# Kernel tuning notes

Hardware: AMD Instinct MI355X
Metric: run time of the kernel (lower is better)

The kernel has to match this reference:

```python
import jax, jax.numpy as jnp
import numpy as np

B, S, E, H = 2, 2048, 1024, 16
D = E // H  # head_dim = 64


def setup_inputs() -> dict:
    key = jax.random.key(0)
    k1, k2, k3 = jax.random.split(key, 3)
    scale_in = 1.0 / np.sqrt(E)
    return {
        "x": jax.random.normal(k1, (B, S, E), dtype=jnp.float32),
        "mask": jnp.ones((B, S), dtype=jnp.int32),
        "qkv_w": jax.random.normal(k2, (3 * E, E), dtype=jnp.float32) * scale_in,
        "qkv_b": jnp.zeros((3 * E,), dtype=jnp.float32),
        "proj_w": jax.random.normal(k3, (E, E), dtype=jnp.float32) * scale_in,
        "proj_b": jnp.zeros((E,), dtype=jnp.float32),
    }


def reference(x, mask, qkv_w, qkv_b, proj_w, proj_b):
    b, s, e = x.shape
    # fused QKV projection: torch Linear -> x @ W^T + b
    qkv = x @ qkv_w.T + qkv_b                      # [B,S,3E]
    qkv = qkv.reshape(b, s, 3, H, D).transpose(2, 0, 3, 1, 4)  # [3,B,H,S,D]
    q, k, v = qkv[0], qkv[1], qkv[2]
    scores = jnp.einsum("bhqd,bhkd->bhqk", q, k) / jnp.sqrt(jnp.float32(D))
    # mask [B,S] -> [B,1,1,S]; masked_fill(mask==0, -inf)
    m = mask[:, None, None, :]
    scores = jnp.where(m == 0, -jnp.inf, scores)
    attn = jax.nn.softmax(scores, axis=-1)
    attn = jnp.nan_to_num(attn, nan=0.0)           # fully-masked rows -> 0
    # dropout is identity in eval mode (deterministic reference)
    out = jnp.einsum("bhqk,bhkd->bhqd", attn, v)   # [B,H,S,D]
    out = out.transpose(0, 2, 1, 3).reshape(b, s, e)
    out = out @ proj_w.T + proj_b
    return out
```

## Files before the change

### kernel.cpp

```cpp
#include <hip/hip_runtime.h>
#include <hip/hip_bf16.h>

#define B_ 2
#define S_ 2048
#define E_ 1024
#define H_ 16
#define D_ 64

typedef __bf16 bf16x8 __attribute__((ext_vector_type(8)));
typedef __bf16 bf16x4 __attribute__((ext_vector_type(4)));
typedef float f32x4 __attribute__((ext_vector_type(4)));


__device__ __forceinline__ f32x4 mfma16(bf16x8 a, bf16x8 b, f32x4 c) {
    return __builtin_amdgcn_mfma_f32_16x16x32_bf16(a, b, c, 0, 0, 0);
}

__device__ __forceinline__ void gl_lds16(const __bf16* g, __bf16* l) {
    __builtin_amdgcn_global_load_lds(
        (const __attribute__((address_space(1))) unsigned int*)g,
        (__attribute__((address_space(3))) unsigned int*)l, 16, 0, 0);
}
__device__ __forceinline__ void gl_lds4(const int* g, int* l) {
    __builtin_amdgcn_global_load_lds(
        (const __attribute__((address_space(1))) unsigned int*)g,
        (__attribute__((address_space(3))) unsigned int*)l, 4, 0, 0);
}

__global__ __launch_bounds__(256) void convert_kernel(
        const float* __restrict__ x, const float* __restrict__ qkvw,
        const float* __restrict__ projw, __bf16* __restrict__ ws) {
    const long NX = 4194304, NW = 3145728;
    long i = (long)(blockIdx.x * 256 + threadIdx.x) * 4;
    const float* src; __bf16* dst; long off;
    if (i < NX)           { src = x;     dst = ws;           off = i; }
    else if (i < NX + NW) { src = qkvw;  dst = ws + NX;      off = i - NX; }
    else                  { src = projw; dst = ws + NX + NW; off = i - NX - NW; }
    float4 v = *(const float4*)(src + off);
    bf16x4 o = { (__bf16)v.x, (__bf16)v.y, (__bf16)v.z, (__bf16)v.w };
    *(bf16x4*)(dst + off) = o;
}

__device__ __forceinline__ void gemm_core_h(
        const __bf16* __restrict__ A, const __bf16* __restrict__ Bm,
        int rowT, int colT, int K,
        __bf16* AT, __bf16* BT, f32x4 acc[2][4]) {
    int tid = threadIdx.x;
    int wave = tid >> 6, lane = tid & 63;
    int quad = lane >> 4, lm = lane & 15;
    int srow = wave * 8 + (lane >> 3);
    int schunk = lane & 7;
    const __bf16* ap = A + (long)(rowT + srow) * K + schunk * 8;
    const __bf16* bp = Bm + (long)(colT + srow) * K + schunk * 8;
    for (int k0 = 0; k0 < K; k0 += 64) {
        __syncthreads();
        for (int i = 0; i < 4; i++)
            gl_lds16(ap + (long)i * 32 * K + k0, AT + (i * 256 + wave * 64) * 8);
        for (int i = 0; i < 2; i++)
            gl_lds16(bp + (long)i * 32 * K + k0, BT + (i * 256 + wave * 64) * 8);
        __syncthreads();
        for (int ks = 0; ks < 2; ks++) {
            bf16x8 af[2], bfr[4];
            for (int m = 0; m < 2; m++)
                af[m] = *(const bf16x8*)(AT + (wave * 32 + m * 16 + lm) * 64 + ks * 32 + quad * 8);
            for (int n = 0; n < 4; n++)
                bfr[n] = *(const bf16x8*)(BT + (n * 16 + lm) * 64 + ks * 32 + quad * 8);
            for (int m = 0; m < 2; m++)
                for (int n = 0; n < 4; n++)
                    acc[m][n] = mfma16(af[m], bfr[n], acc[m][n]);
        }
    }
}

#define C1 0.18033688011112043f

__global__ __launch_bounds__(512, 2) void qkv_gemm(
        const __bf16* __restrict__ xbf, const __bf16* __restrict__ wbf,
        const float* __restrict__ bias, __bf16* __restrict__ qk,
        __bf16* __restrict__ vt) {
    __shared__ __align__(16) __bf16 Ab[3][256 * 32];
    __shared__ __align__(16) __bf16 Bb[3][256 * 32];
    int tid = threadIdx.x;
    int wave = tid >> 6, lane = tid & 63;
    int quad = lane >> 4, lm = lane & 15;
    int wr = wave >> 2, wc = wave & 3;
    int rowT = blockIdx.x * 256, colT = blockIdx.y * 256;
    int r16 = lane >> 2, c4 = lane & 3;
    int cs = c4 ^ ((r16 >> 1) & 3);
    const __bf16* asrc = xbf + (long)(rowT + wave * 32 + r16) * E_ + cs * 8;
    const __bf16* bsrc = wbf + (long)(colT + wave * 32 + r16) * E_ + cs * 8;
    int xr = quad ^ ((lm >> 1) & 3);

    f32x4 acc[8][4] = {};

#define STAGE_QKV(buf, k0) { \
    gl_lds16(asrc + (k0),           &Ab[buf][(wave * 32) * 32]); \
    gl_lds16(asrc + 16 * E_ + (k0), &Ab[buf][(wave * 32 + 16) * 32]); \
    gl_lds16(bsrc + (k0),           &Bb[buf][(wave * 32) * 32]); \
    gl_lds16(bsrc + 16 * E_ + (k0), &Bb[buf][(wave * 32 + 16) * 32]); }

    STAGE_QKV(0, 0)
    STAGE_QKV(1, 32)
    asm volatile("s_waitcnt vmcnt(4)" ::: "memory");
    __builtin_amdgcn_sched_barrier(0);
    __builtin_amdgcn_s_barrier();
    __builtin_amdgcn_sched_barrier(0);

    #pragma unroll
    for (int k = 0; k < 32; k++) {
        const int cur = k % 3;
        bf16x8 a[8], bfr[4];
        #pragma unroll
        for (int m = 0; m < 8; m++)
            a[m] = *(const bf16x8*)(&Ab[cur][(wr * 128 + m * 16 + lm) * 32 + xr * 8]);
        #pragma unroll
        for (int n = 0; n < 4; n++)
            bfr[n] = *(const bf16x8*)(&Bb[cur][(wc * 64 + n * 16 + lm) * 32 + xr * 8]);
        asm volatile("s_waitcnt lgkmcnt(0)" ::: "memory");
        __builtin_amdgcn_sched_barrier(0);
        __builtin_amdgcn_s_barrier();
        __builtin_amdgcn_sched_barrier(0);
        if (k < 30) STAGE_QKV((k + 2) % 3, (k + 2) * 32)
        __builtin_amdgcn_s_setprio(1);
        #pragma unroll
        for (int m = 0; m < 8; m++)
            #pragma unroll
            for (int n = 0; n < 4; n++)
                acc[m][n] = mfma16(a[m], bfr[n], acc[m][n]);
        __builtin_amdgcn_s_setprio(0);
        if (k < 30) { asm volatile("s_waitcnt vmcnt(4)" ::: "memory"); }
        else        { asm volatile("s_waitcnt vmcnt(0)" ::: "memory"); }
        __builtin_amdgcn_sched_barrier(0);
        __builtin_amdgcn_s_barrier();
        __builtin_amdgcn_sched_barrier(0);
    }
#undef STAGE_QKV

    int which = colT >> 10;
    if (which < 2) {
        float sc = which ? 1.f : C1;
        #pragma unroll
        for (int n = 0; n < 4; n++) {
            int col = colT + wc * 64 + n * 16 + lm;
            float bv = bias[col];
            int rem = col & 1023;
            int h = rem >> 6, d = rem & 63;
            #pragma unroll
            for (int m = 0; m < 8; m++) {
                int rowb = rowT + wr * 128 + m * 16 + quad * 4;
                for (int r = 0; r < 4; r++) {
                    int row = rowb + r;
                    int b = row >> 11, s = row & 2047;
                    float v = (acc[m][n][r] + bv) * sc;
                    qk[(long)((which * B_ + b) * H_ + h) * (S_ * D_) + (long)s * D_ + d] = (__bf16)v;
                }
            }
        }
    } else {
        #pragma unroll
        for (int n = 0; n < 4; n++) {
            int col = colT + wc * 64 + n * 16 + lm;
            float bv = bias[col];
            int mr = col & 1023;
            int h = mr >> 6, d = mr & 63;
            #pragma unroll
            for (int m = 0; m < 8; m++) {
                int row = rowT + wr * 128 + m * 16 + quad * 4;
                int b = row >> 11, s = row & 2047;
                bf16x4 o = { (__bf16)(acc[m][n][0] + bv), (__bf16)(acc[m][n][1] + bv),
                             (__bf16)(acc[m][n][2] + bv), (__bf16)(acc[m][n][3] + bv) };
                *(bf16x4*)(vt + (long)((b * H_ + h) * D_ + d) * S_ + s) = o;
            }
        }
    }
}

__global__ __launch_bounds__(512, 2) void flash_attn(
        const __bf16* __restrict__ qk, const __bf16* __restrict__ vt,
        const int* __restrict__ mask, __bf16* __restrict__ attn) {
    int wave = threadIdx.x >> 6, lane = threadIdx.x & 63;
    int quad = lane >> 4, lm = lane & 15;
    int bh = blockIdx.x;
    int qb = blockIdx.y;
    int b = bh >> 4, h = bh & 15;
    const long BHSD = (long)B_ * H_ * S_ * D_;
    const __bf16* qp  = qk + (long)bh * (S_ * D_);
    const __bf16* kp  = qk + BHSD + (long)bh * (S_ * D_);
    const __bf16* vtp = vt + (long)bh * (D_ * S_);
    const int* mrow = mask + b * S_;

    __shared__ __align__(16) __bf16 Kl[2][128 * 64];
    __shared__ __align__(16) __bf16 Vl[2][64 * 128];
    __shared__ __align__(16) int    Ml[2][128];
    __shared__ __align__(16) __bf16 Plds[8][2][16][136];

    int q0[2];
    q0[0] = qb * 256 + wave * 32;
    q0[1] = q0[0] + 16;
    bf16x8 qa[2][2];
    for (int t = 0; t < 2; t++)
        for (int x = 0; x < 2; x++)
            qa[t][x] = *(const bf16x8*)(qp + (long)(q0[t] + lm) * D_ + x * 32 + quad * 8);

    f32x4 O[2][4] = {};
    f32x4 Ol[2] = {};
    bf16x8 ones8;
    for (int j = 0; j < 8; j++) ones8[j] = (__bf16)1.0f;

    struct __align__(8) bfx4 { __hip_bfloat162 lo, hi; };

    int r8 = lane >> 3, c8 = lane & 7;
    int cs = c8 ^ r8;
    int xs = lm & 7;

    {
        #pragma unroll
        for (int j = 0; j < 2; j++) {
            int wp = wave * 2 + j;
            int krow = wp * 8 + r8;
            gl_lds16(kp + (long)krow * 64 + cs * 8, &Kl[0][wp * 512]);
            int vrow = wp * 4 + quad;
            int vcs = lm ^ (vrow & 15);
            gl_lds16(vtp + (long)vrow * S_ + vcs * 8, &Vl[0][wp * 512]);
        }
        if (wave == 0) {
            gl_lds4(mrow + lane, &Ml[0][0]);
            gl_lds4(mrow + 64 + lane, &Ml[0][64]);
        }
    }
    __syncthreads();

    for (int i = 0; i < 16; i++) {
        int bs = i & 1;
        if (i < 15) {
            int kb1 = (i + 1) * 128;
            #pragma unroll
            for (int j = 0; j < 2; j++) {
                int wp = wave * 2 + j;
                int krow = wp * 8 + r8;
                gl_lds16(kp + (long)(kb1 + krow) * 64 + cs * 8, &Kl[bs ^ 1][wp * 512]);
                int vrow = wp * 4 + quad;
                int vcs = lm ^ (vrow & 15);
                gl_lds16(vtp + (long)vrow * S_ + kb1 + vcs * 8, &Vl[bs ^ 1][wp * 512]);
            }
            if (wave == 0) {
                gl_lds4(mrow + kb1 + lane, &Ml[bs ^ 1][0]);
                gl_lds4(mrow + kb1 + 64 + lane, &Ml[bs ^ 1][64]);
            }
        }
        const __bf16* Kb = &Kl[bs][0];
        #pragma unroll
        for (int g = 0; g < 4; g++) {
            bf16x8 kf[2][2];
            f32x4 zsel[2];
            #pragma unroll
            for (int j = 0; j < 2; j++) {
                int hh = g * 2 + j;
                int row = hh * 16 + lm;
                kf[j][0] = *(const bf16x8*)(Kb + row * 64 + ((quad ^ xs) << 3));
                kf[j][1] = *(const bf16x8*)(Kb + row * 64 + (((4 + quad) ^ xs) << 3));
                int4 mq = *(const int4*)(&Ml[bs][hh * 16 + quad * 4]);
                zsel[j][0] = mq.x ? -32.f : -1e38f;
                zsel[j][1] = mq.y ? -32.f : -1e38f;
                zsel[j][2] = mq.z ? -32.f : -1e38f;
                zsel[j][3] = mq.w ? -32.f : -1e38f;
            }
            f32x4 st[2][2];
            __builtin_amdgcn_s_setprio(1);
            #pragma unroll
            for (int j = 0; j < 2; j++)
                #pragma unroll
                for (int t = 0; t < 2; t++) {
                    f32x4 z = mfma16(kf[j][0], qa[t][0], zsel[j]);
                    st[j][t] = mfma16(kf[j][1], qa[t][1], z);
                }
            __builtin_amdgcn_s_setprio(0);
            #pragma unroll
            for (int j = 0; j < 2; j++)
                #pragma unroll
                for (int t = 0; t < 2; t++) {
                    int hh = g * 2 + j;
                    float e0 = __builtin_amdgcn_exp2f(st[j][t][0]);
                    float e1 = __builtin_amdgcn_exp2f(st[j][t][1]);
                    float e2 = __builtin_amdgcn_exp2f(st[j][t][2]);
                    float e3 = __builtin_amdgcn_exp2f(st[j][t][3]);
                    bfx4 pk;
                    pk.lo = __float22bfloat162_rn(float2{e0, e1});
                    pk.hi = __float22bfloat162_rn(float2{e2, e3});
                    *(bfx4*)(&Plds[wave][t][lm][hh * 16 + quad * 4]) = pk;
                }
        }
        const __bf16* Vb = &Vl[bs][0];
        #pragma unroll
        for (int x = 0; x < 4; x++) {
            bf16x8 vf[4];
            #pragma unroll
            for (int c = 0; c < 4; c++) {
                int row = c * 16 + lm;
                vf[c] = *(const bf16x8*)(Vb + row * 128 + (((x * 4 + quad) ^ lm) << 3));
            }
            bf16x8 pa[2];
            #pragma unroll
            for (int t = 0; t < 2; t++)
                pa[t] = *(const bf16x8*)(&Plds[wave][t][lm][x * 32 + quad * 8]);
            __builtin_amdgcn_s_setprio(1);
            #pragma unroll
            for (int t = 0; t < 2; t++) {
                #pragma unroll
                for (int c = 0; c < 4; c++)
                    O[t][c] = mfma16(pa[t], vf[c], O[t][c]);
                Ol[t] = mfma16(pa[t], ones8, Ol[t]);
            }
            __builtin_amdgcn_s_setprio(0);
        }
        __syncthreads();
    }

    for (int t = 0; t < 2; t++)
        for (int r = 0; r < 4; r++) {
            float lb = Ol[t][r];
            float inv = lb > 0.f ? 1.f / lb : 0.f;
            int s = q0[t] + quad * 4 + r;
            for (int c = 0; c < 4; c++) {
                int e = h * 64 + c * 16 + lm;
                attn[(long)(b * S_ + s) * E_ + e] = (__bf16)(O[t][c][r] * inv);
            }
        }
}

__global__ __launch_bounds__(256, 2) void proj_gemm(
        const __bf16* __restrict__ abf, const __bf16* __restrict__ wbf,
        const float* __restrict__ bias, float* __restrict__ out) {
    __shared__ __align__(16) __bf16 AT[128 * 64];
    __shared__ __align__(16) __bf16 BT[64 * 64];
    f32x4 acc[2][4] = {};
    int rowT = blockIdx.x * 128, colT = blockIdx.y * 64;
    gemm_core_h(abf, wbf, rowT, colT, E_, AT, BT, acc);
    int wave = threadIdx.x >> 6, lane = threadIdx.x & 63;
    int quad = lane >> 4, lm = lane & 15;
    for (int n = 0; n < 4; n++) {
        int col = colT + n * 16 + lm;
        float bv = bias[col];
        for (int m = 0; m < 2; m++) {
            int rowb = rowT + wave * 32 + m * 16 + quad * 4;
            for (int r = 0; r < 4; r++) {
                int row = rowb + r;
                out[(long)row * E_ + col] = acc[m][n][r] + bv;
            }
        }
    }
}

extern "C" void kernel_launch(void* const* d_in, const int* in_sizes, int n_in,
                              void* d_out, int out_size, void* d_ws, size_t ws_size,
                              hipStream_t stream) {
    const float* x      = (const float*)d_in[0];
    const int*   mask   = (const int*)d_in[1];
    const float* qkv_w  = (const float*)d_in[2];
    const float* qkv_b  = (const float*)d_in[3];
    const float* proj_w = (const float*)d_in[4];
    const float* proj_b = (const float*)d_in[5];
    float* out = (float*)d_out;
    __bf16* ws = (__bf16*)d_ws;

    __bf16* x_bf     = ws;
    __bf16* qkvw_bf  = ws + 4194304;
    __bf16* projw_bf = ws + 7340032;
    __bf16* qk_bf    = ws + 8388608;
    __bf16* vt_bf    = ws + 16777216;
    __bf16* attn_bf  = ws + 20971520;

    convert_kernel<<<8192, 256, 0, stream>>>(x, qkv_w, proj_w, ws);
    qkv_gemm<<<dim3(16, 12), 512, 0, stream>>>(x_bf, qkvw_bf, qkv_b, qk_bf, vt_bf);
    flash_attn<<<dim3(32, 8), 512, 0, stream>>>(qk_bf, vt_bf, mask, attn_bf);
    proj_gemm<<<dim3(32, 16), 256, 0, stream>>>(attn_bf, projw_bf, proj_b, out);
}
```

Before: 188.2 us.

## Split QKV GEMM k-step into two MFMA halves interleaved with staged loads

```diff
diff --git a/kernel.cpp b/kernel.cpp
--- a/kernel.cpp
+++ b/kernel.cpp
@@ -93,48 +93,71 @@
 
     f32x4 acc[8][4] = {};
 
-#define STAGE_QKV(buf, k0) { \
+#define STAGE_A(buf, k0) { \
     gl_lds16(asrc + (k0),           &Ab[buf][(wave * 32) * 32]); \
-    gl_lds16(asrc + 16 * E_ + (k0), &Ab[buf][(wave * 32 + 16) * 32]); \
+    gl_lds16(asrc + 16 * E_ + (k0), &Ab[buf][(wave * 32 + 16) * 32]); }
+#define STAGE_B(buf, k0) { \
     gl_lds16(bsrc + (k0),           &Bb[buf][(wave * 32) * 32]); \
     gl_lds16(bsrc + 16 * E_ + (k0), &Bb[buf][(wave * 32 + 16) * 32]); }
 
-    STAGE_QKV(0, 0)
-    STAGE_QKV(1, 32)
+    STAGE_A(0, 0)  STAGE_B(0, 0)
+    STAGE_A(1, 32) STAGE_B(1, 32)
     asm volatile("s_waitcnt vmcnt(4)" ::: "memory");
     __builtin_amdgcn_sched_barrier(0);
     __builtin_amdgcn_s_barrier();
-    __builtin_amdgcn_sched_barrier(0);
-
-    #pragma unroll
-    for (int k = 0; k < 32; k++) {
-        const int cur = k % 3;
-        bf16x8 a[8], bfr[4];
-        #pragma unroll
-        for (int m = 0; m < 8; m++)
-            a[m] = *(const bf16x8*)(&Ab[cur][(wr * 128 + m * 16 + lm) * 32 + xr * 8]);
-        #pragma unroll
-        for (int n = 0; n < 4; n++)
-            bfr[n] = *(const bf16x8*)(&Bb[cur][(wc * 64 + n * 16 + lm) * 32 + xr * 8]);
-        asm volatile("s_waitcnt lgkmcnt(0)" ::: "memory");
-        __builtin_amdgcn_sched_barrier(0);
-        __builtin_amdgcn_s_barrier();
-        __builtin_amdgcn_sched_barrier(0);
-        if (k < 30) STAGE_QKV((k + 2) % 3, (k + 2) * 32)
-        __builtin_amdgcn_s_setprio(1);
-        #pragma unroll
-        for (int m = 0; m < 8; m++)
-            #pragma unroll
-            for (int n = 0; n < 4; n++)
-                acc[m][n] = mfma16(a[m], bfr[n], acc[m][n]);
-        __builtin_amdgcn_s_setprio(0);
-        if (k < 30) { asm volatile("s_waitcnt vmcnt(4)" ::: "memory"); }
-        else        { asm volatile("s_waitcnt vmcnt(0)" ::: "memory"); }
-        __builtin_amdgcn_sched_barrier(0);
-        __builtin_amdgcn_s_barrier();
-        __builtin_amdgcn_sched_barrier(0);
-    }
-#undef STAGE_QKV
+
+#define QKV_STEP(KK, CUR, NXT, SON) { \
+    bf16x8 a0[4], b0[4]; \
+    _Pragma("unroll") \
+    for (int m = 0; m < 4; m++) \
+        a0[m] = *(const bf16x8*)(&Ab[CUR][(wr * 128 + m * 16 + lm) * 32 + xr * 8]); \
+    _Pragma("unroll") \
+    for (int n = 0; n < 4; n++) \
+        b0[n] = *(const bf16x8*)(&Bb[CUR][(wc * 64 + n * 16 + lm) * 32 + xr * 8]); \
+    if (SON) STAGE_A(NXT, (KK + 2) * 32) \
+    __builtin_amdgcn_s_barrier(); \
+    asm volatile("s_waitcnt lgkmcnt(0)" ::: "memory"); \
+    __builtin_amdgcn_sched_barrier(0); \
+    __builtin_amdgcn_s_setprio(1); \
+    _Pragma("unroll") \
+    for (int m = 0; m < 4; m++) \
+        _Pragma("unroll") \
+        for (int n = 0; n < 4; n++) \
+            acc[m][n] = mfma16(a0[m], b0[n], acc[m][n]); \
+    __builtin_amdgcn_s_setprio(0); \
+    __builtin_amdgcn_s_barrier(); \
+    bf16x8 a1[4]; \
+    _Pragma("unroll") \
+    for (int m = 0; m < 4; m++) \
+        a1[m] = *(const bf16x8*)(&Ab[CUR][(wr * 128 + 64 + m * 16 + lm) * 32 + xr * 8]); \
+    if (SON) STAGE_B(NXT, (KK + 2) * 32) \
+    __builtin_amdgcn_s_barrier(); \
+    asm volatile("s_waitcnt lgkmcnt(0)" ::: "memory"); \
+    __builtin_amdgcn_sched_barrier(0); \
+    __builtin_amdgcn_s_setprio(1); \
+    _Pragma("unroll") \
+    for (int m = 0; m < 4; m++) \
+        _Pragma("unroll") \
+        for (int n = 0; n < 4; n++) \
+            acc[4 + m][n] = mfma16(a1[m], b0[n], acc[4 + m][n]); \
+    __builtin_amdgcn_s_setprio(0); \
+    if (SON) { asm volatile("s_waitcnt vmcnt(4)" ::: "memory"); } \
+    else     { asm volatile("s_waitcnt vmcnt(0)" ::: "memory"); } \
+    __builtin_amdgcn_sched_barrier(0); \
+    __builtin_amdgcn_s_barrier(); \
+}
+
+    for (int j = 0; j < 10; j++) {
+        int k0 = j * 3;
+        QKV_STEP(k0,     0, 2, 1)
+        QKV_STEP(k0 + 1, 1, 0, 1)
+        QKV_STEP(k0 + 2, 2, 1, 1)
+    }
+    QKV_STEP(30, 0, 2, 0)
+    QKV_STEP(31, 1, 0, 0)
+#undef QKV_STEP
+#undef STAGE_A
+#undef STAGE_B
 
     int which = colT >> 10;
     if (which < 2) {
```

New measurement: 194.0 us. 3.0% more time.
